# Kernel optimization log

Measured on AMD Instinct MI355X. Metric: run time of the kernel, lower is better.

## Reference

```python
import jax, jax.numpy as jnp
import numpy as np

B, S, E, H = 2, 2048, 1024, 16
DH = E // H  # 64


def setup_inputs() -> dict:
    key = jax.random.key(0)
    ks = jax.random.split(key, 13)
    s = 1.0 / np.sqrt(E)
    inp = {
        'query': jax.random.normal(ks[0], (B, S, E), jnp.float32),
        'key':   jax.random.normal(ks[1], (B, S, E), jnp.float32),
        'value': jax.random.normal(ks[2], (B, S, E), jnp.float32),
        # nn.Linear weights stored [out, in]
        'Wq': jax.random.uniform(ks[3], (E, E), jnp.float32, -s, s),
        'bq': jax.random.uniform(ks[4], (E,), jnp.float32, -s, s),
        'Wk': jax.random.uniform(ks[5], (E, E), jnp.float32, -s, s),
        'bk': jax.random.uniform(ks[6], (E,), jnp.float32, -s, s),
        'Wv': jax.random.uniform(ks[7], (E, E), jnp.float32, -s, s),
        'bv': jax.random.uniform(ks[8], (E,), jnp.float32, -s, s),
        # 1x1 Conv2d over head channels: weight [H, H] (squeezed from [H,H,1,1]), bias [H]
        'Wc': jax.random.uniform(ks[9], (H, H), jnp.float32, -1.0 / np.sqrt(H), 1.0 / np.sqrt(H)),
        'bc': jax.random.uniform(ks[10], (H,), jnp.float32, -1.0 / np.sqrt(H), 1.0 / np.sqrt(H)),
        'Wo': jax.random.uniform(ks[11], (E, E), jnp.float32, -s, s),
        'bo': jax.random.uniform(ks[12], (E,), jnp.float32, -s, s),
    }
    return inp


def reference(query, key, value, Wq, bq, Wk, bk, Wv, bv, Wc, bc, Wo, bo):
    b, s = query.shape[0], query.shape[1]
    # projections -> (B, H, S, Dh)
    def split_heads(x):
        return x.reshape(b, s, H, DH).transpose(0, 2, 1, 3)
    Q = split_heads(query @ Wq.T + bq)
    K = split_heads(key @ Wk.T + bk)
    V = split_heads(value @ Wv.T + bv)
    # raw scores (B, H, S, S)
    scores = jnp.einsum('bhqd,bhkd->bhqk', Q, K) / np.sqrt(DH).astype(np.float32)
    # 1x1 conv mixes logits across heads: channel-wise matmul + bias
    noise = jnp.einsum('gh,bhqk->bgqk', Wc, scores) + bc[None, :, None, None]
    scores = scores + noise
    weights = jax.nn.softmax(scores, axis=-1)
    out = jnp.einsum('bhqk,bhkd->bhqd', weights, V)  # (B, H, S, Dh)
    out = out.transpose(0, 2, 1, 3).reshape(b, s, E)
    return out @ Wo.T + bo
```

## Files before the change

### kernel.cpp

```cpp
#include <hip/hip_runtime.h>


typedef __attribute__((ext_vector_type(8))) short bf16x8_t;
typedef __attribute__((ext_vector_type(4))) short bf16x4_t;
typedef __attribute__((ext_vector_type(4))) float f32x4_t;

__device__ inline unsigned short f2bf(float f) {
  unsigned u = __builtin_bit_cast(unsigned, f);
  u += 0x7fffu + ((u >> 16) & 1u);
  return (unsigned short)(u >> 16);
}

#define GLOAD(dst, ptr) \
  asm volatile("global_load_dwordx4 %0, %1, off" : "=v"(dst) : "v"((const void*)(ptr)))
#define WAITV0() { asm volatile("s_waitcnt vmcnt(0)"); __builtin_amdgcn_sched_barrier(0); }

__device__ inline void bar_lds() {
  asm volatile("s_waitcnt lgkmcnt(0)" ::: "memory");
  __builtin_amdgcn_s_barrier();
}

struct ConvArgs {
  const float* src[7];
  unsigned short* dst[7];
  int n[7];
};

__global__ __launch_bounds__(256) void convert_f32_bf16(ConvArgs a) {
  const int which = blockIdx.y;
  const int i = (blockIdx.x * 256 + threadIdx.x) * 8;
  if (i >= a.n[which]) return;
  const float* s = a.src[which] + i;
  f32x4_t x0 = *(const f32x4_t*)(s);
  f32x4_t x1 = *(const f32x4_t*)(s + 4);
  bf16x8_t o;
#pragma unroll
  for (int j = 0; j < 4; j++) o[j] = (short)f2bf(x0[j]);
#pragma unroll
  for (int j = 0; j < 4; j++) o[4 + j] = (short)f2bf(x1[j]);
  *(bf16x8_t*)(a.dst[which] + i) = o;
}

struct GemmArgs {
  const unsigned short* A[3];
  const unsigned short* Bt[3];
  const float* bias[3];
  void* C[3];
  int f32out[3];
};

__global__ __launch_bounds__(256) void gemm_bt(GemmArgs ga, int M, int N, int K)
{
  __shared__ unsigned short As[128 * 32];
  __shared__ unsigned short Bs[128 * 32];
  const int z = blockIdx.z;
  const unsigned short* __restrict__ A  = ga.A[z];
  const unsigned short* __restrict__ Bt = ga.Bt[z];
  const float* __restrict__ bias = ga.bias[z];
  void* __restrict__ C = ga.C[z];
  const int f32out = ga.f32out[z];

  const int t = threadIdx.x;
  const int l = t & 63;
  const int w = t >> 6;
  const int quad = l >> 4, n16 = l & 15;
  const int wm = (w & 1) * 64, wn = (w >> 1) * 64;
  const long m0 = (long)blockIdx.x * 128, n0 = (long)blockIdx.y * 128;

  f32x4_t acc[4][4] = {};

  const unsigned short* gA = A + (m0 + (t >> 2)) * (long)K + (t & 3) * 8;
  const unsigned short* gB = Bt + (n0 + (t >> 2)) * (long)K + (t & 3) * 8;
  const long rowskip = 64l * K;

  bf16x8_t ra0, ra1, rb0, rb1;
  GLOAD(ra0, gA);            GLOAD(ra1, gA + rowskip);
  GLOAD(rb0, gB);            GLOAD(rb1, gB + rowskip);
  WAITV0();

  for (int kt = 0; kt < K; kt += 32) {
    bar_lds();
    *(bf16x8_t*)&As[t * 8] = ra0;
    *(bf16x8_t*)&As[2048 + t * 8] = ra1;
    *(bf16x8_t*)&Bs[t * 8] = rb0;
    *(bf16x8_t*)&Bs[2048 + t * 8] = rb1;
    bar_lds();
    const long ktn = (kt + 32 < K) ? kt + 32 : 0;
    GLOAD(ra0, gA + ktn);      GLOAD(ra1, gA + ktn + rowskip);
    GLOAD(rb0, gB + ktn);      GLOAD(rb1, gB + ktn + rowskip);

    bf16x8_t af[4], bfr[4];
#pragma unroll
    for (int i = 0; i < 4; i++) {
      af[i]  = *(const bf16x8_t*)&As[(wm + i * 16 + n16) * 32 + quad * 8];
      bfr[i] = *(const bf16x8_t*)&Bs[(wn + i * 16 + n16) * 32 + quad * 8];
    }
#pragma unroll
    for (int mi = 0; mi < 4; mi++)
#pragma unroll
      for (int ni = 0; ni < 4; ni++)
        acc[mi][ni] = __builtin_amdgcn_mfma_f32_16x16x32_bf16(af[mi], bfr[ni], acc[mi][ni], 0, 0, 0);
    WAITV0();
  }

#pragma unroll
  for (int ni = 0; ni < 4; ni++) {
    const long n = n0 + wn + ni * 16 + n16;
    const float bv = bias[n];
#pragma unroll
    for (int mi = 0; mi < 4; mi++) {
#pragma unroll
      for (int r = 0; r < 4; r++) {
        const long m = m0 + wm + mi * 16 + quad * 4 + r;
        const float v = acc[mi][ni][r] + bv;
        if (f32out) ((float*)C)[m * N + n] = v;
        else ((unsigned short*)C)[m * N + n] = f2bf(v);
      }
    }
  }
}

__global__ __launch_bounds__(256) void transpose_v(
    const unsigned short* __restrict__ V, unsigned short* __restrict__ VT)
{
  __shared__ unsigned short tile[64][72];
  const int t = threadIdx.x;
  const int s0 = blockIdx.x * 64, h = blockIdx.y, b = blockIdx.z;
#pragma unroll
  for (int r = 0; r < 2; r++) {
    const int elem = r * 2048 + t * 8;
    const int s = elem >> 6, d = elem & 63;
    *(bf16x8_t*)&tile[s][d] =
        *(const bf16x8_t*)&V[(size_t)(b * 2048 + s0 + s) * 1024 + h * 64 + d];
  }
  __syncthreads();
#pragma unroll
  for (int r = 0; r < 2; r++) {
    const int elem = r * 2048 + t * 8;
    const int d = elem >> 6, sl = elem & 63;
    bf16x8_t o;
#pragma unroll
    for (int j = 0; j < 8; j++) o[j] = (short)tile[sl + j][d];
    *(bf16x8_t*)&VT[((size_t)(b * 16 + h) * 64 + d) * 2048 + s0 + sl] = o;
  }
}

__global__ __launch_bounds__(1024, 4) void attention_fused(
    const unsigned short* __restrict__ Qb, const unsigned short* __restrict__ Kb,
    const unsigned short* __restrict__ VT, const float* __restrict__ Wc,
    unsigned short* __restrict__ Obuf)
{
  __shared__ unsigned short sraw[2][512 * 36];
  __shared__ unsigned short pbuf[2][16 * 580];
  __shared__ float lbuf[16 * 17];
  __shared__ unsigned short mmat[256];

  const int t = threadIdx.x;
  const int g = t >> 6, l = t & 63;
  const int quad = l >> 4, n16 = l & 15;

  const int id = blockIdx.x;
  const int xcd = id & 7;
  const int b = xcd >> 2;
  const int qb = (xcd & 3) * 32 + (id >> 3);
  const int q0 = qb * 16;

  for (int i = t; i < 2 * 512 * 36; i += 1024) (&sraw[0][0])[i] = 0;
  if (t < 256) {
    const float v = ((((t >> 4) == (t & 15)) ? 1.0f : 0.0f) + Wc[t]) * 0.1803368801111204f;
    mmat[t] = f2bf(v);
  }
  __syncthreads();

  bf16x8_t mfrag;
  if (quad < 2) mfrag = *(const bf16x8_t*)&mmat[n16 * 16 + quad * 8];
  else { bf16x8_t z = {0, 0, 0, 0, 0, 0, 0, 0}; mfrag = z; }
  const int c7 = g >> 2;

  bf16x8_t qf[2];
#pragma unroll
  for (int dr = 0; dr < 2; dr++)
    qf[dr] = *(const bf16x8_t*)&Qb[(size_t)(b * 2048 + q0 + n16) * 1024 + g * 64 + dr * 32 + quad * 8];

  const int slot = g ^ (quad << 3);
  const unsigned short* kptr = Kb + (size_t)(b * 2048 + n16) * 1024 + g * 64 + quad * 8;
  const unsigned short* vptr = VT + ((size_t)(b * 16 + g) * 64 + n16) * 2048 + quad * 8;

  bf16x8_t kf[2][2], vf[4];
  auto load_kf = [&](int kt) {
#pragma unroll
    for (int kc = 0; kc < 2; kc++)
#pragma unroll
      for (int dr = 0; dr < 2; dr++)
        kf[kc][dr] = *(const bf16x8_t*)(kptr + (size_t)(kt + kc * 16) * 1024 + dr * 32);
  };
  auto load_vf = [&](int kt) {
#pragma unroll
    for (int dc = 0; dc < 4; dc++)
      vf[dc] = *(const bf16x8_t*)(vptr + (size_t)dc * 16 * 2048 + kt);
  };
  auto qk_stage = [&](unsigned short* dst) {
    f32x4_t sf[2] = {};
#pragma unroll
    for (int kc = 0; kc < 2; kc++)
#pragma unroll
      for (int dr = 0; dr < 2; dr++)
        sf[kc] = __builtin_amdgcn_mfma_f32_16x16x32_bf16(qf[dr], kf[kc][dr], sf[kc], 0, 0, 0);
#pragma unroll
    for (int kc = 0; kc < 2; kc++)
#pragma unroll
      for (int r = 0; r < 4; r++)
        dst[((quad * 4 + r) * 32 + kc * 16 + n16) * 36 + slot] = f2bf(sf[kc][r]);
  };

  load_kf(0);
  qk_stage(&sraw[0][0]);
  load_kf(32);
  __syncthreads();

  f32x4_t o[4] = {};
  float l_run = 0.0f;

  for (int it = 0; it < 64; ++it) {
    const int cur = it & 1;
    const int oth = cur ^ 1;

    if (it > 0) {
      const unsigned short* pp = &pbuf[oth][g * 580 + n16 * 36 + quad * 8];
      bf16x4_t plo = *(const bf16x4_t*)pp;
      bf16x4_t phi = *(const bf16x4_t*)(pp + 4);
      bf16x8_t pf = {plo[0], plo[1], plo[2], plo[3], phi[0], phi[1], phi[2], phi[3]};
#pragma unroll
      for (int dc = 0; dc < 4; dc++)
        o[dc] = __builtin_amdgcn_mfma_f32_16x16x32_bf16(pf, vf[dc], o[dc], 0, 0, 0);
    }
    load_vf(it * 32);

    f32x4_t mixd[2];
#pragma unroll
    for (int c2 = 0; c2 < 2; c2++) {
      const int c = g * 2 + c2;
      const unsigned short* sp = &sraw[cur][(c * 16 + n16) * 36 + ((quad ^ c7) << 3)];
      bf16x4_t lo = *(const bf16x4_t*)sp;
      bf16x4_t hi = *(const bf16x4_t*)(sp + 4);
      bf16x8_t aa = {lo[0], lo[1], lo[2], lo[3], hi[0], hi[1], hi[2], hi[3]};
      f32x4_t z = {};
      mixd[c2] = __builtin_amdgcn_mfma_f32_16x16x32_bf16(aa, mfrag, z, 0, 0, 0);
    }

    float p[2][4];
    float lsum = 0.0f;
#pragma unroll
    for (int c2 = 0; c2 < 2; c2++)
#pragma unroll
      for (int r = 0; r < 4; r++) {
        p[c2][r] = exp2f(mixd[c2][r]);
        lsum += p[c2][r];
      }
    l_run += lsum;

    const int pbase = n16 * 580 + g * 36 + quad * 4;
#pragma unroll
    for (int c2 = 0; c2 < 2; c2++)
#pragma unroll
      for (int rp = 0; rp < 2; rp++) {
        unsigned pk;
        asm("v_cvt_pk_bf16_f32 %0, %1, %2"
            : "=v"(pk) : "v"(p[c2][2 * rp]), "v"(p[c2][2 * rp + 1]));
        *(unsigned*)&pbuf[cur][pbase + c2 * 16 + 2 * rp] = pk;
      }

    if (it < 63) qk_stage(&sraw[oth][0]);
    if (it < 62) load_kf((it + 2) * 32);

    __syncthreads();
  }

  {
    const unsigned short* pp = &pbuf[1][g * 580 + n16 * 36 + quad * 8];
    bf16x4_t plo = *(const bf16x4_t*)pp;
    bf16x4_t phi = *(const bf16x4_t*)(pp + 4);
    bf16x8_t pf = {plo[0], plo[1], plo[2], plo[3], phi[0], phi[1], phi[2], phi[3]};
#pragma unroll
    for (int dc = 0; dc < 4; dc++)
      o[dc] = __builtin_amdgcn_mfma_f32_16x16x32_bf16(pf, vf[dc], o[dc], 0, 0, 0);
  }

  l_run += __shfl_xor(l_run, 16);
  l_run += __shfl_xor(l_run, 32);
  if (quad == 0) lbuf[n16 * 17 + g] = l_run;
  __syncthreads();
  float linv[4];
#pragma unroll
  for (int r = 0; r < 4; r++) linv[r] = 1.0f / lbuf[g * 17 + quad * 4 + r];
#pragma unroll
  for (int dc = 0; dc < 4; dc++)
#pragma unroll
    for (int r = 0; r < 4; r++) {
      const float v = o[dc][r] * linv[r];
      Obuf[(size_t)(b * 2048 + q0 + quad * 4 + r) * 1024 + g * 64 + dc * 16 + n16] = f2bf(v);
    }
}

extern "C" void kernel_launch(void* const* d_in, const int* in_sizes, int n_in,
                              void* d_out, int out_size, void* d_ws, size_t ws_size,
                              hipStream_t stream) {
  const float* query = (const float*)d_in[0];
  const float* key   = (const float*)d_in[1];
  const float* value = (const float*)d_in[2];
  const float* Wq = (const float*)d_in[3];
  const float* bq = (const float*)d_in[4];
  const float* Wk = (const float*)d_in[5];
  const float* bk = (const float*)d_in[6];
  const float* Wv = (const float*)d_in[7];
  const float* bv = (const float*)d_in[8];
  const float* Wc = (const float*)d_in[9];
  const float* Wo = (const float*)d_in[11];
  const float* bo = (const float*)d_in[12];

  char* ws = (char*)d_ws;
  const size_t MB = 1024 * 1024;
  unsigned short* q_bf  = (unsigned short*)(ws);
  unsigned short* k_bf  = (unsigned short*)(ws + 8 * MB);
  unsigned short* v_bf  = (unsigned short*)(ws + 16 * MB);
  unsigned short* wq_bf = (unsigned short*)(ws + 24 * MB);
  unsigned short* wk_bf = (unsigned short*)(ws + 26 * MB);
  unsigned short* wv_bf = (unsigned short*)(ws + 28 * MB);
  unsigned short* wo_bf = (unsigned short*)(ws + 30 * MB);
  unsigned short* Qb    = (unsigned short*)(ws + 32 * MB);
  unsigned short* Kb    = (unsigned short*)(ws + 40 * MB);
  unsigned short* Vb    = (unsigned short*)(ws + 48 * MB);
  unsigned short* VT   = k_bf;
  unsigned short* Obuf = q_bf;

  ConvArgs ca;
  ca.src[0] = query; ca.dst[0] = q_bf;  ca.n[0] = 2 * 2048 * 1024;
  ca.src[1] = key;   ca.dst[1] = k_bf;  ca.n[1] = 2 * 2048 * 1024;
  ca.src[2] = value; ca.dst[2] = v_bf;  ca.n[2] = 2 * 2048 * 1024;
  ca.src[3] = Wq;    ca.dst[3] = wq_bf; ca.n[3] = 1024 * 1024;
  ca.src[4] = Wk;    ca.dst[4] = wk_bf; ca.n[4] = 1024 * 1024;
  ca.src[5] = Wv;    ca.dst[5] = wv_bf; ca.n[5] = 1024 * 1024;
  ca.src[6] = Wo;    ca.dst[6] = wo_bf; ca.n[6] = 1024 * 1024;
  convert_f32_bf16<<<dim3(2048, 7), 256, 0, stream>>>(ca);

  GemmArgs g3;
  g3.A[0] = q_bf; g3.Bt[0] = wq_bf; g3.bias[0] = bq; g3.C[0] = Qb; g3.f32out[0] = 0;
  g3.A[1] = k_bf; g3.Bt[1] = wk_bf; g3.bias[1] = bk; g3.C[1] = Kb; g3.f32out[1] = 0;
  g3.A[2] = v_bf; g3.Bt[2] = wv_bf; g3.bias[2] = bv; g3.C[2] = Vb; g3.f32out[2] = 0;
  gemm_bt<<<dim3(32, 8, 3), 256, 0, stream>>>(g3, 4096, 1024, 1024);

  transpose_v<<<dim3(32, 16, 2), 256, 0, stream>>>(Vb, VT);

  attention_fused<<<dim3(256), 1024, 0, stream>>>(Qb, Kb, VT, Wc, Obuf);

  GemmArgs g1;
  g1.A[0] = Obuf; g1.Bt[0] = wo_bf; g1.bias[0] = bo; g1.C[0] = d_out; g1.f32out[0] = 1;
  g1.A[1] = g1.A[0]; g1.Bt[1] = g1.Bt[0]; g1.bias[1] = g1.bias[0]; g1.C[1] = g1.C[0]; g1.f32out[1] = 1;
  g1.A[2] = g1.A[0]; g1.Bt[2] = g1.Bt[0]; g1.bias[2] = g1.bias[0]; g1.C[2] = g1.C[0]; g1.f32out[2] = 1;
  gemm_bt<<<dim3(32, 8, 1), 256, 0, stream>>>(g1, 4096, 1024, 1024);
}
```

Before: 427.2 us.

## Split attention along key dimension into two halves and merge partial sums

The attention kernel now splits the 2048-key range into two halves, launching 512 blocks instead of 256, and writes unnormalized fp32 partial outputs and row sums to workspace. A new merge kernel adds the halves, normalizes, and converts to bf16. The LDS double buffering is dropped for a single buffer with an extra barrier per iteration, and launch bounds request more blocks per CU. This is meant to fill more CUs, at the cost of extra fp32 global traffic, another kernel launch, and less overlap inside the loop.

```diff
diff --git a/kernel.cpp b/kernel.cpp
--- a/kernel.cpp
+++ b/kernel.cpp
@@ -145,14 +145,13 @@
   }
 }
 
-__global__ __launch_bounds__(1024, 4) void attention_fused(
+__global__ __launch_bounds__(1024, 8) void attention_fused(
     const unsigned short* __restrict__ Qb, const unsigned short* __restrict__ Kb,
     const unsigned short* __restrict__ VT, const float* __restrict__ Wc,
-    unsigned short* __restrict__ Obuf)
+    float* __restrict__ Op0, float* __restrict__ Op1, float* __restrict__ Ll)
 {
-  __shared__ unsigned short sraw[2][512 * 36];
-  __shared__ unsigned short pbuf[2][16 * 580];
-  __shared__ float lbuf[16 * 17];
+  __shared__ unsigned short sraw[512 * 36];
+  __shared__ unsigned short pbuf[16 * 580];
   __shared__ unsigned short mmat[256];
 
   const int t = threadIdx.x;
@@ -162,10 +161,12 @@
   const int id = blockIdx.x;
   const int xcd = id & 7;
   const int b = xcd >> 2;
-  const int qb = (xcd & 3) * 32 + (id >> 3);
+  const int kb = (xcd >> 1) & 1;
+  const int qb = (xcd & 1) * 64 + (id >> 3);
   const int q0 = qb * 16;
-
-  for (int i = t; i < 2 * 512 * 36; i += 1024) (&sraw[0][0])[i] = 0;
+  const int k0 = kb * 1024;
+
+  for (int i = t; i < 512 * 36; i += 1024) sraw[i] = 0;
   if (t < 256) {
     const float v = ((((t >> 4) == (t & 15)) ? 1.0f : 0.0f) + Wc[t]) * 0.1803368801111204f;
     mmat[t] = f2bf(v);
@@ -183,8 +184,8 @@
     qf[dr] = *(const bf16x8_t*)&Qb[(size_t)(b * 2048 + q0 + n16) * 1024 + g * 64 + dr * 32 + quad * 8];
 
   const int slot = g ^ (quad << 3);
-  const unsigned short* kptr = Kb + (size_t)(b * 2048 + n16) * 1024 + g * 64 + quad * 8;
-  const unsigned short* vptr = VT + ((size_t)(b * 16 + g) * 64 + n16) * 2048 + quad * 8;
+  const unsigned short* kptr = Kb + (size_t)(b * 2048 + k0 + n16) * 1024 + g * 64 + quad * 8;
+  const unsigned short* vptr = VT + ((size_t)(b * 16 + g) * 64 + n16) * 2048 + k0 + quad * 8;
 
   bf16x8_t kf[2][2], vf[4];
   auto load_kf = [&](int kt) {
@@ -199,7 +200,7 @@
     for (int dc = 0; dc < 4; dc++)
       vf[dc] = *(const bf16x8_t*)(vptr + (size_t)dc * 16 * 2048 + kt);
   };
-  auto qk_stage = [&](unsigned short* dst) {
+  auto qk_stage = [&]() {
     f32x4_t sf[2] = {};
 #pragma unroll
     for (int kc = 0; kc < 2; kc++)
@@ -210,37 +211,26 @@
     for (int kc = 0; kc < 2; kc++)
 #pragma unroll
       for (int r = 0; r < 4; r++)
-        dst[((quad * 4 + r) * 32 + kc * 16 + n16) * 36 + slot] = f2bf(sf[kc][r]);
+        sraw[((quad * 4 + r) * 32 + kc * 16 + n16) * 36 + slot] = f2bf(sf[kc][r]);
   };
 
   load_kf(0);
-  qk_stage(&sraw[0][0]);
-  load_kf(32);
-  __syncthreads();
+  qk_stage();
 
   f32x4_t o[4] = {};
   float l_run = 0.0f;
 
-  for (int it = 0; it < 64; ++it) {
-    const int cur = it & 1;
-    const int oth = cur ^ 1;
-
-    if (it > 0) {
-      const unsigned short* pp = &pbuf[oth][g * 580 + n16 * 36 + quad * 8];
-      bf16x4_t plo = *(const bf16x4_t*)pp;
-      bf16x4_t phi = *(const bf16x4_t*)(pp + 4);
-      bf16x8_t pf = {plo[0], plo[1], plo[2], plo[3], phi[0], phi[1], phi[2], phi[3]};
-#pragma unroll
-      for (int dc = 0; dc < 4; dc++)
-        o[dc] = __builtin_amdgcn_mfma_f32_16x16x32_bf16(pf, vf[dc], o[dc], 0, 0, 0);
-    }
-    load_vf(it * 32);
+  for (int it = 0; it < 32; ++it) {
+    const int kt = it * 32;
+    __syncthreads();
+
+    load_vf(kt);
 
     f32x4_t mixd[2];
 #pragma unroll
     for (int c2 = 0; c2 < 2; c2++) {
       const int c = g * 2 + c2;
-      const unsigned short* sp = &sraw[cur][(c * 16 + n16) * 36 + ((quad ^ c7) << 3)];
+      const unsigned short* sp = &sraw[(c * 16 + n16) * 36 + ((quad ^ c7) << 3)];
       bf16x4_t lo = *(const bf16x4_t*)sp;
       bf16x4_t hi = *(const bf16x4_t*)(sp + 4);
       bf16x8_t aa = {lo[0], lo[1], lo[2], lo[3], hi[0], hi[1], hi[2], hi[3]};
@@ -267,39 +257,62 @@
         unsigned pk;
         asm("v_cvt_pk_bf16_f32 %0, %1, %2"
             : "=v"(pk) : "v"(p[c2][2 * rp]), "v"(p[c2][2 * rp + 1]));
-        *(unsigned*)&pbuf[cur][pbase + c2 * 16 + 2 * rp] = pk;
+        *(unsigned*)&pbuf[pbase + c2 * 16 + 2 * rp] = pk;
       }
 
-    if (it < 63) qk_stage(&sraw[oth][0]);
-    if (it < 62) load_kf((it + 2) * 32);
-
     __syncthreads();
-  }
-
-  {
-    const unsigned short* pp = &pbuf[1][g * 580 + n16 * 36 + quad * 8];
-    bf16x4_t plo = *(const bf16x4_t*)pp;
-    bf16x4_t phi = *(const bf16x4_t*)(pp + 4);
-    bf16x8_t pf = {plo[0], plo[1], plo[2], plo[3], phi[0], phi[1], phi[2], phi[3]};
-#pragma unroll
-    for (int dc = 0; dc < 4; dc++)
-      o[dc] = __builtin_amdgcn_mfma_f32_16x16x32_bf16(pf, vf[dc], o[dc], 0, 0, 0);
+
+    {
+      const unsigned short* pp = &pbuf[g * 580 + n16 * 36 + quad * 8];
+      bf16x4_t plo = *(const bf16x4_t*)pp;
+      bf16x4_t phi = *(const bf16x4_t*)(pp + 4);
+      bf16x8_t pf = {plo[0], plo[1], plo[2], plo[3], phi[0], phi[1], phi[2], phi[3]};
+#pragma unroll
+      for (int dc = 0; dc < 4; dc++)
+        o[dc] = __builtin_amdgcn_mfma_f32_16x16x32_bf16(pf, vf[dc], o[dc], 0, 0, 0);
+    }
+
+    if (it < 31) {
+      load_kf(kt + 32);
+      qk_stage();
+    }
   }
 
   l_run += __shfl_xor(l_run, 16);
   l_run += __shfl_xor(l_run, 32);
-  if (quad == 0) lbuf[n16 * 17 + g] = l_run;
-  __syncthreads();
-  float linv[4];
-#pragma unroll
-  for (int r = 0; r < 4; r++) linv[r] = 1.0f / lbuf[g * 17 + quad * 4 + r];
+  if (quad == 0)
+    Ll[((size_t)(kb * 2 + b) * 16 + n16) * 2048 + q0 + g] = l_run;
+  float* const ob = kb ? Op1 : Op0;
 #pragma unroll
   for (int dc = 0; dc < 4; dc++)
 #pragma unroll
-    for (int r = 0; r < 4; r++) {
-      const float v = o[dc][r] * linv[r];
-      Obuf[(size_t)(b * 2048 + q0 + quad * 4 + r) * 1024 + g * 64 + dc * 16 + n16] = f2bf(v);
-    }
+    for (int r = 0; r < 4; r++)
+      ob[((size_t)(b * 2048 + q0 + quad * 4 + r)) * 1024 + g * 64 + dc * 16 + n16] = o[dc][r];
+}
+
+__global__ __launch_bounds__(256) void merge_halves(
+    const float* __restrict__ Op0, const float* __restrict__ Op1,
+    const float* __restrict__ Ll, unsigned short* __restrict__ Obuf)
+{
+  const int i = blockIdx.x * 256 + threadIdx.x;
+  const size_t e8 = (size_t)i * 8;
+  const int e = (int)(e8 & 1023);
+  const int q = (int)((e8 >> 10) & 2047);
+  const int b = (int)(e8 >> 21);
+  const int h = e >> 6;
+  const size_t row = (size_t)b * 2048 + q;
+  const size_t mi = ((size_t)b * 16 + h) * 2048 + q;
+  const float s = 1.0f / (Ll[mi] + Ll[2 * 16 * 2048 + mi]);
+  const float* pa = Op0 + row * 1024 + e;
+  const float* pb = Op1 + row * 1024 + e;
+  f32x4_t a0 = *(const f32x4_t*)pa, a1 = *(const f32x4_t*)(pa + 4);
+  f32x4_t b0 = *(const f32x4_t*)pb, b1 = *(const f32x4_t*)(pb + 4);
+  bf16x8_t o8;
+#pragma unroll
+  for (int j = 0; j < 4; j++) o8[j] = (short)f2bf((a0[j] + b0[j]) * s);
+#pragma unroll
+  for (int j = 0; j < 4; j++) o8[4 + j] = (short)f2bf((a1[j] + b1[j]) * s);
+  *(bf16x8_t*)&Obuf[row * 1024 + e] = o8;
 }
 
 extern "C" void kernel_launch(void* const* d_in, const int* in_sizes, int n_in,
@@ -330,6 +343,9 @@
   unsigned short* Qb    = (unsigned short*)(ws + 32 * MB);
   unsigned short* Kb    = (unsigned short*)(ws + 40 * MB);
   unsigned short* Vb    = (unsigned short*)(ws + 48 * MB);
+  float* Op0 = (float*)(ws + 56 * MB);
+  float* Ll  = (float*)(ws + 72 * MB);
+  float* Op1 = (float*)d_out;
   unsigned short* VT   = k_bf;
   unsigned short* Obuf = q_bf;
 
@@ -351,7 +367,9 @@
 
   transpose_v<<<dim3(32, 16, 2), 256, 0, stream>>>(Vb, VT);
 
-  attention_fused<<<dim3(256), 1024, 0, stream>>>(Qb, Kb, VT, Wc, Obuf);
+  attention_fused<<<dim3(512), 1024, 0, stream>>>(Qb, Kb, VT, Wc, Op0, Op1, Ll);
+
+  merge_halves<<<dim3(2048), 256, 0, stream>>>(Op0, Op1, Ll, Obuf);
 
   GemmArgs g1;
   g1.A[0] = Obuf; g1.Bt[0] = wo_bf; g1.bias[0] = bo; g1.C[0] = d_out; g1.f32out[0] = 1;
```

Result: slower. 505.4 us (+18.3%).

## Widen key tile to 64 and drop LDS double buffering in fused attention

Applied to the files above, without the earlier changes.

Doubles the key block handled per iteration from 32 to 64, halving the loop trip count and the number of block-wide barriers. It removes the double-buffered score and probability LDS arrays in favour of single buffers with two barriers per iteration, and reorders work so PV runs right after the softmax store and the next QK stage follows. This cuts barrier and loop overhead per key, but raises register pressure (twice the K/V fragments) and loses the overlap the double buffers gave between QK, the head mix and PV.

```diff
diff --git a/kernel.cpp b/kernel.cpp
--- a/kernel.cpp
+++ b/kernel.cpp
@@ -150,8 +150,8 @@
     const unsigned short* __restrict__ VT, const float* __restrict__ Wc,
     unsigned short* __restrict__ Obuf)
 {
-  __shared__ unsigned short sraw[2][512 * 36];
-  __shared__ unsigned short pbuf[2][16 * 580];
+  __shared__ unsigned short sraw[1024 * 36];
+  __shared__ unsigned short pbuf[16 * 1092];
   __shared__ float lbuf[16 * 17];
   __shared__ unsigned short mmat[256];
 
@@ -165,7 +165,7 @@
   const int qb = (xcd & 3) * 32 + (id >> 3);
   const int q0 = qb * 16;
 
-  for (int i = t; i < 2 * 512 * 36; i += 1024) (&sraw[0][0])[i] = 0;
+  for (int i = t; i < 1024 * 36; i += 1024) sraw[i] = 0;
   if (t < 256) {
     const float v = ((((t >> 4) == (t & 15)) ? 1.0f : 0.0f) + Wc[t]) * 0.1803368801111204f;
     mmat[t] = f2bf(v);
@@ -186,10 +186,10 @@
   const unsigned short* kptr = Kb + (size_t)(b * 2048 + n16) * 1024 + g * 64 + quad * 8;
   const unsigned short* vptr = VT + ((size_t)(b * 16 + g) * 64 + n16) * 2048 + quad * 8;
 
-  bf16x8_t kf[2][2], vf[4];
+  bf16x8_t kf[4][2], vf[4][2];
   auto load_kf = [&](int kt) {
 #pragma unroll
-    for (int kc = 0; kc < 2; kc++)
+    for (int kc = 0; kc < 4; kc++)
 #pragma unroll
       for (int dr = 0; dr < 2; dr++)
         kf[kc][dr] = *(const bf16x8_t*)(kptr + (size_t)(kt + kc * 16) * 1024 + dr * 32);
@@ -197,50 +197,42 @@
   auto load_vf = [&](int kt) {
 #pragma unroll
     for (int dc = 0; dc < 4; dc++)
-      vf[dc] = *(const bf16x8_t*)(vptr + (size_t)dc * 16 * 2048 + kt);
+#pragma unroll
+      for (int kc2 = 0; kc2 < 2; kc2++)
+        vf[dc][kc2] = *(const bf16x8_t*)(vptr + (size_t)dc * 16 * 2048 + kt + kc2 * 32);
   };
-  auto qk_stage = [&](unsigned short* dst) {
-    f32x4_t sf[2] = {};
-#pragma unroll
-    for (int kc = 0; kc < 2; kc++)
+  auto qk_stage = [&]() {
+    f32x4_t sf[4] = {};
+#pragma unroll
+    for (int kc = 0; kc < 4; kc++)
 #pragma unroll
       for (int dr = 0; dr < 2; dr++)
         sf[kc] = __builtin_amdgcn_mfma_f32_16x16x32_bf16(qf[dr], kf[kc][dr], sf[kc], 0, 0, 0);
 #pragma unroll
-    for (int kc = 0; kc < 2; kc++)
+    for (int kc = 0; kc < 4; kc++)
 #pragma unroll
       for (int r = 0; r < 4; r++)
-        dst[((quad * 4 + r) * 32 + kc * 16 + n16) * 36 + slot] = f2bf(sf[kc][r]);
+        sraw[((quad * 4 + r) * 64 + kc * 16 + n16) * 36 + slot] = f2bf(sf[kc][r]);
   };
 
   load_kf(0);
-  qk_stage(&sraw[0][0]);
-  load_kf(32);
-  __syncthreads();
+  qk_stage();
 
   f32x4_t o[4] = {};
   float l_run = 0.0f;
 
-  for (int it = 0; it < 64; ++it) {
-    const int cur = it & 1;
-    const int oth = cur ^ 1;
-
-    if (it > 0) {
-      const unsigned short* pp = &pbuf[oth][g * 580 + n16 * 36 + quad * 8];
-      bf16x4_t plo = *(const bf16x4_t*)pp;
-      bf16x4_t phi = *(const bf16x4_t*)(pp + 4);
-      bf16x8_t pf = {plo[0], plo[1], plo[2], plo[3], phi[0], phi[1], phi[2], phi[3]};
-#pragma unroll
-      for (int dc = 0; dc < 4; dc++)
-        o[dc] = __builtin_amdgcn_mfma_f32_16x16x32_bf16(pf, vf[dc], o[dc], 0, 0, 0);
-    }
-    load_vf(it * 32);
-
-    f32x4_t mixd[2];
-#pragma unroll
-    for (int c2 = 0; c2 < 2; c2++) {
-      const int c = g * 2 + c2;
-      const unsigned short* sp = &sraw[cur][(c * 16 + n16) * 36 + ((quad ^ c7) << 3)];
+  for (int it = 0; it < 32; ++it) {
+    const int kt = it * 64;
+    __syncthreads();
+
+    load_vf(kt);
+    if (it < 31) load_kf(kt + 64);
+
+    f32x4_t mixd[4];
+#pragma unroll
+    for (int c2 = 0; c2 < 4; c2++) {
+      const int c = g * 4 + c2;
+      const unsigned short* sp = &sraw[(c * 16 + n16) * 36 + ((quad ^ c7) << 3)];
       bf16x4_t lo = *(const bf16x4_t*)sp;
       bf16x4_t hi = *(const bf16x4_t*)(sp + 4);
       bf16x8_t aa = {lo[0], lo[1], lo[2], lo[3], hi[0], hi[1], hi[2], hi[3]};
@@ -248,10 +240,10 @@
       mixd[c2] = __builtin_amdgcn_mfma_f32_16x16x32_bf16(aa, mfrag, z, 0, 0, 0);
     }
 
-    float p[2][4];
+    float p[4][4];
     float lsum = 0.0f;
 #pragma unroll
-    for (int c2 = 0; c2 < 2; c2++)
+    for (int c2 = 0; c2 < 4; c2++)
 #pragma unroll
       for (int r = 0; r < 4; r++) {
         p[c2][r] = exp2f(mixd[c2][r]);
@@ -259,31 +251,30 @@
       }
     l_run += lsum;
 
-    const int pbase = n16 * 580 + g * 36 + quad * 4;
-#pragma unroll
-    for (int c2 = 0; c2 < 2; c2++)
-#pragma unroll
-      for (int rp = 0; rp < 2; rp++) {
-        unsigned pk;
-        asm("v_cvt_pk_bf16_f32 %0, %1, %2"
-            : "=v"(pk) : "v"(p[c2][2 * rp]), "v"(p[c2][2 * rp + 1]));
-        *(unsigned*)&pbuf[cur][pbase + c2 * 16 + 2 * rp] = pk;
-      }
-
-    if (it < 63) qk_stage(&sraw[oth][0]);
-    if (it < 62) load_kf((it + 2) * 32);
+#pragma unroll
+    for (int c2 = 0; c2 < 4; c2++) {
+      const int pb_ = n16 * 1092 + g * 68 + c2 * 16 + quad * 4;
+      unsigned pk0, pk1;
+      asm("v_cvt_pk_bf16_f32 %0, %1, %2" : "=v"(pk0) : "v"(p[c2][0]), "v"(p[c2][1]));
+      asm("v_cvt_pk_bf16_f32 %0, %1, %2" : "=v"(pk1) : "v"(p[c2][2]), "v"(p[c2][3]));
+      *(unsigned*)&pbuf[pb_] = pk0;
+      *(unsigned*)&pbuf[pb_ + 2] = pk1;
+    }
 
     __syncthreads();
-  }
-
-  {
-    const unsigned short* pp = &pbuf[1][g * 580 + n16 * 36 + quad * 8];
-    bf16x4_t plo = *(const bf16x4_t*)pp;
-    bf16x4_t phi = *(const bf16x4_t*)(pp + 4);
-    bf16x8_t pf = {plo[0], plo[1], plo[2], plo[3], phi[0], phi[1], phi[2], phi[3]};
-#pragma unroll
-    for (int dc = 0; dc < 4; dc++)
-      o[dc] = __builtin_amdgcn_mfma_f32_16x16x32_bf16(pf, vf[dc], o[dc], 0, 0, 0);
+
+#pragma unroll
+    for (int kc2 = 0; kc2 < 2; kc2++) {
+      const unsigned short* pp = &pbuf[g * 1092 + n16 * 68 + kc2 * 32 + quad * 8];
+      bf16x4_t plo = *(const bf16x4_t*)pp;
+      bf16x4_t phi = *(const bf16x4_t*)(pp + 4);
+      bf16x8_t pf = {plo[0], plo[1], plo[2], plo[3], phi[0], phi[1], phi[2], phi[3]};
+#pragma unroll
+      for (int dc = 0; dc < 4; dc++)
+        o[dc] = __builtin_amdgcn_mfma_f32_16x16x32_bf16(pf, vf[dc][kc2], o[dc], 0, 0, 0);
+    }
+
+    if (it < 31) qk_stage();
   }
 
   l_run += __shfl_xor(l_run, 16);
```

After: 437.8 us. +2.5%, slower.
